# Optimization experiments

Measured on AMD Instinct MI355X. Metric: run time of the kernel, lower is better.

Reference implementation:

```python
import jax, jax.numpy as jnp
import numpy as np

HIDDEN = 1024
HEADS = 16
HEAD_DIM = HIDDEN // HEADS
BATCH = 1
SEQ = 4096
SCALE = 1.0 / np.sqrt(HEAD_DIM)


def setup_inputs() -> dict:
    key = jax.random.key(0)
    ks = jax.random.split(key, 5)
    s = 0.02
    return {
        "hidden_states": jax.random.normal(ks[0], (BATCH, SEQ, HIDDEN), jnp.float32),
        "qkv_w": jax.random.normal(ks[1], (3 * HIDDEN, HIDDEN), jnp.float32) * s,
        "qkv_b": jax.random.normal(ks[2], (3 * HIDDEN,), jnp.float32) * s,
        "out_w": jax.random.normal(ks[3], (HIDDEN, HIDDEN), jnp.float32) * s,
        "out_b": jax.random.normal(ks[4], (HIDDEN,), jnp.float32) * s,
    }


def reference(hidden_states, qkv_w, qkv_b, out_w, out_b):
    B, S, H = hidden_states.shape
    # fused QKV projection (torch Linear: x @ W^T + b)
    qkv = hidden_states @ qkv_w.T + qkv_b              # [B, S, 3H]
    qkv = qkv.reshape(B, S, 3, HEADS, HEAD_DIM)
    qkv = jnp.transpose(qkv, (2, 0, 3, 1, 4))          # [3, B, nh, S, hd]
    q, k, v = qkv[0] * SCALE, qkv[1], qkv[2]
    # ring attention over all KV chunks == full softmax attention
    scores = jnp.einsum('bhqd,bhkd->bhqk', q, k)       # [B, nh, S, S]
    probs = jax.nn.softmax(scores, axis=-1)
    ctx = jnp.einsum('bhqk,bhkd->bhqd', probs, v)      # [B, nh, S, hd]
    ctx = jnp.transpose(ctx, (0, 2, 1, 3)).reshape(B, S, H)
    return ctx @ out_w.T + out_b
```

## Files before the change

### kernel.cpp

```cpp
#include <hip/hip_runtime.h>

#define SEQ 4096
#define HID 1024
#define NHEADS 16
#define HDIM 64
#define QK_SCALE 0.1803368801111204f

typedef float  f32x4 __attribute__((ext_vector_type(4)));
typedef int    i32x4 __attribute__((ext_vector_type(4)));
typedef int    i32x2 __attribute__((ext_vector_type(2)));
typedef __bf16 bf16x8 __attribute__((ext_vector_type(8)));
typedef unsigned short u16;
typedef unsigned int   u32;

static __device__ __forceinline__ u16 f2bf(float f) {
  u32 u = __builtin_bit_cast(u32, f);
  return (u16)((u + 0x7FFFu + ((u >> 16) & 1u)) >> 16);
}
static __device__ __forceinline__ int cvtpk(float lo, float hi) {
  int r;
  asm("v_cvt_pk_bf16_f32 %0, %1, %2" : "=v"(r) : "v"(lo), "v"(hi));
  return r;
}
static __device__ __forceinline__ f32x4 exp2v(f32x4 x) {
  f32x4 o;
  o.x = __builtin_amdgcn_exp2f(x.x);
  o.y = __builtin_amdgcn_exp2f(x.y);
  o.z = __builtin_amdgcn_exp2f(x.z);
  o.w = __builtin_amdgcn_exp2f(x.w);
  return o;
}
static __device__ __forceinline__ float sum4(f32x4 x) {
  return (x.x + x.y) + (x.z + x.w);
}
static __device__ __forceinline__ f32x4 mfma16(i32x4 a, i32x4 b, f32x4 c) {
  return __builtin_amdgcn_mfma_f32_16x16x32_bf16(
      __builtin_bit_cast(bf16x8, a), __builtin_bit_cast(bf16x8, b), c, 0, 0, 0);
}

#define GLD(gsrc, lds_dst)                                        \
  __builtin_amdgcn_global_load_lds(                               \
      (const __attribute__((address_space(1))) void*)(gsrc),      \
      (__attribute__((address_space(3))) void*)(lds_dst), 16, 0, 0)

__global__ __launch_bounds__(256) void cvt_kernel(
    const float* __restrict__ X, const float* __restrict__ Wq,
    const float* __restrict__ Wo, u16* __restrict__ Xb,
    u16* __restrict__ Wqb, u16* __restrict__ Wob) {
  const int u = blockIdx.x * 256 + threadIdx.x;
  const float* src; u16* dst; int local;
  if (u < 524288)       { src = X;  dst = Xb;  local = u; }
  else if (u < 917504)  { src = Wq; dst = Wqb; local = u - 524288; }
  else                  { src = Wo; dst = Wob; local = u - 917504; }
  const int row = local >> 7, gu = local & 127;
  const int w = gu & 7, blk = gu >> 3;
  const int ks = w >> 2, q2 = w & 3;
  const float* s = src + (size_t)row * 1024 + blk * 64 + ks * 32 + q2 * 4;
  float4 x0 = *(const float4*)s;
  float4 x1 = *(const float4*)(s + 16);
  i32x4 o = {cvtpk(x0.x, x0.y), cvtpk(x0.z, x0.w),
             cvtpk(x1.x, x1.y), cvtpk(x1.z, x1.w)};
  *(i32x4*)(dst + (size_t)row * 1024 + blk * 64 + w * 8) = o;
}

static __device__ __forceinline__ void gemm_tile(
    const u16* __restrict__ A, const u16* __restrict__ B,
    int mb, int nb, u16 (*LA)[128][64], u16 (*LB)[128][64],
    f32x4 acc[4][4]) {
  const int t = threadIdx.x, lane = t & 63, wv = t >> 6;
  const int g = lane >> 4, r = lane & 15;
  const int wr = wv >> 1, wc = wv & 1;
  const int lr = lane >> 3, sl = lane & 7;

  const u16* pa = A + (size_t)(mb + wv * 32 + lr) * 1024 + ((sl ^ lr) << 3);
  const u16* pb = B + (size_t)(nb + wv * 32 + lr) * 1024 + ((sl ^ lr) << 3);

  const u16* afp[4][2];
  const u16* bfp[4][2];
#pragma unroll
  for (int i = 0; i < 4; ++i)
#pragma unroll
    for (int ks = 0; ks < 2; ++ks) {
      const int sw = r & 7;
      afp[i][ks] = &LA[0][wr * 64 + i * 16 + r][(((ks * 4 + g) ^ sw) << 3)];
      bfp[i][ks] = &LB[0][wc * 64 + i * 16 + r][(((ks * 4 + g) ^ sw) << 3)];
    }
#pragma unroll
  for (int i = 0; i < 4; ++i)
#pragma unroll
    for (int j = 0; j < 4; ++j) acc[i][j] = (f32x4)0.0f;

#pragma unroll
  for (int j = 0; j < 4; ++j) {
    GLD(pa + j * 8 * 1024, &LA[0][wv * 32 + j * 8][0]);
    GLD(pb + j * 8 * 1024, &LB[0][wv * 32 + j * 8][0]);
  }
  pa += 64; pb += 64;
  __syncthreads();

#define GEMM_STEP(BU, PRE)                                                  \
  {                                                                         \
    if (PRE) {                                                              \
      _Pragma("unroll")                                                     \
      for (int j = 0; j < 4; ++j) {                                         \
        GLD(pa + j * 8 * 1024, &LA[(BU) ^ 1][wv * 32 + j * 8][0]);          \
        GLD(pb + j * 8 * 1024, &LB[(BU) ^ 1][wv * 32 + j * 8][0]);          \
      }                                                                     \
      pa += 64; pb += 64;                                                   \
    }                                                                       \
    i32x4 af[4][2], bf[4][2];                                               \
    _Pragma("unroll")                                                       \
    for (int i = 0; i < 4; ++i)                                             \
      _Pragma("unroll")                                                     \
      for (int ks = 0; ks < 2; ++ks) {                                      \
        af[i][ks] = *(const i32x4*)(afp[i][ks] + (BU) * 8192);              \
        bf[i][ks] = *(const i32x4*)(bfp[i][ks] + (BU) * 8192);              \
      }                                                                     \
    __builtin_amdgcn_s_setprio(1);                                          \
    _Pragma("unroll")                                                       \
    for (int ks = 0; ks < 2; ++ks)                                          \
      _Pragma("unroll")                                                     \
      for (int i = 0; i < 4; ++i)                                           \
        _Pragma("unroll")                                                   \
        for (int j = 0; j < 4; ++j)                                         \
          acc[i][j] = mfma16(af[i][ks], bf[j][ks], acc[i][j]);              \
    __builtin_amdgcn_s_setprio(0);                                          \
    __syncthreads();                                                        \
  }

  for (int kk = 0; kk < 8; ++kk) {
    GEMM_STEP(0, true)
    GEMM_STEP(1, (kk < 7))
  }
#undef GEMM_STEP
}

__global__ __launch_bounds__(256) void qkv_kernel(
    const u16* __restrict__ A, const u16* __restrict__ Bw,
    const float* __restrict__ BI, u16* __restrict__ qws,
    u16* __restrict__ kws, u16* __restrict__ vtws) {
  __shared__ u16 LA[2][128][64];
  __shared__ u16 LB[2][128][64];
  const int t = threadIdx.x, lane = t & 63, wv = t >> 6;
  const int g = lane >> 4, r = lane & 15;
  const int wr = wv >> 1, wc = wv & 1;
  const int mb = blockIdx.x * 128, nb = blockIdx.y * 128;

  f32x4 acc[4][4];
  gemm_tile(A, Bw, mb, nb, LA, LB, acc);

#pragma unroll
  for (int ni = 0; ni < 4; ni++) {
    const int n = nb + wc * 64 + ni * 16 + r;
    const float bias = BI[n];
    const int which = n >> 10;
    const int h = (n >> 6) & 15;
    const int d = n & 63;
    if (which == 2) {
      u16* base = vtws + (((size_t)(h * 64 + d)) << 12) + mb + wr * 64;
#pragma unroll
      for (int mi = 0; mi < 4; mi++) {
#pragma unroll
        for (int e = 0; e < 4; e += 2) {
          float v0 = acc[mi][ni][e] + bias;
          float v1 = acc[mi][ni][e + 1] + bias;
          const int s6 = mi * 16 + g * 4 + e;
          const int pos = (s6 & 32) | (((s6 >> 2) & 3) << 3) |
                          (((s6 >> 4) & 1) << 2) | (s6 & 3);
          *(u32*)(base + pos) = (u32)cvtpk(v0, v1);
        }
      }
    } else {
      u16* dst = which ? kws : qws;
      const float sc = which ? 1.0f : QK_SCALE;
      const int dq = ((d & 32) | (((d >> 2) & 3) << 3) |
                      (((d >> 4) & 1) << 2) | (d & 3));
#pragma unroll
      for (int mi = 0; mi < 4; mi++) {
        const int m0 = mb + wr * 64 + mi * 16 + g * 4;
#pragma unroll
        for (int e = 0; e < 4; e += 2) {
          float v0 = (acc[mi][ni][e] + bias) * sc;
          float v1 = (acc[mi][ni][e + 1] + bias) * sc;
          int w = cvtpk(v0, v1);
          dst[((size_t)h * SEQ + m0 + e) * HDIM + dq] = (u16)w;
          dst[((size_t)h * SEQ + m0 + e + 1) * HDIM + dq] = (u16)(w >> 16);
        }
      }
    }
  }
}

__global__ __launch_bounds__(256, 2) void attn_kernel(
    const u16* __restrict__ qws, const u16* __restrict__ kws,
    const u16* __restrict__ vtws, u16* __restrict__ ctx) {
  __shared__ u16 Kl[2][64][64];
  __shared__ u16 Vtl[2][64][64];
  const int t = threadIdx.x;
  const int lane = t & 63, wv = t >> 6;
  const int g = lane >> 4, r = lane & 15;

  const int fb = blockIdx.x;
  const int swz = (fb & 7) * 64 + (fb >> 3);
  const int h = swz >> 5;
  const int qb = (swz & 31) * 128 + wv * 32;

  i32x4 qf[2][2];
#pragma unroll
  for (int qt = 0; qt < 2; qt++)
#pragma unroll
    for (int db = 0; db < 2; db++)
      qf[qt][db] = *(const i32x4*)(qws +
          ((size_t)(h * SEQ + qb + qt * 16 + r) * HDIM + db * 32 + g * 8));

  f32x4 acc[2][4];
  f32x4 l4[2];
  const f32x4 zero4 = (f32x4)0.0f;
#pragma unroll
  for (int qt = 0; qt < 2; qt++) {
    l4[qt] = (f32x4)0.0f;
#pragma unroll
    for (int dc = 0; dc < 4; dc++) acc[qt][dc] = (f32x4)0.0f;
  }

  const u16* kh_base = kws + (size_t)h * SEQ * HDIM;
  const u16* vt_base = vtws + ((size_t)h << 18);

  const int lr8 = lane >> 3, sl = lane & 7;
  const u16* kgA = kh_base + (size_t)(16 * wv + lr8) * HDIM +
                   ((sl ^ (lr8 & 7)) << 3);
  const u16* kgB = kgA + 8 * HDIM;
  const u16* vtgA = vt_base + (size_t)(16 * wv + lr8) * SEQ +
                    ((sl ^ (lr8 & 7)) << 3);
  const u16* vtgB = vtgA + (size_t)8 * SEQ;

  const u16* kfp0[4];
  const u16* kfp1[4];
  const u16* vfp0[4];
  const u16* vfp1[4];
#pragma unroll
  for (int i = 0; i < 4; ++i) {
    const int R = i * 16 + r;
    const int sw = R & 7;
    kfp0[i] = &Kl[0][R][(g ^ sw) << 3];
    kfp1[i] = &Kl[0][R][((4 + g) ^ sw) << 3];
    vfp0[i] = &Vtl[0][R][(g ^ sw) << 3];
    vfp1[i] = &Vtl[0][R][((4 + g) ^ sw) << 3];
  }

  GLD(kgA, &Kl[0][wv * 16][0]);
  GLD(kgB, &Kl[0][wv * 16 + 8][0]);
  GLD(vtgA, &Vtl[0][wv * 16][0]);
  GLD(vtgB, &Vtl[0][wv * 16 + 8][0]);
  kgA += 4096; kgB += 4096; vtgA += 64; vtgB += 64;
  __syncthreads();

#define ATTN_STEP(B, PRE)                                                   \
  {                                                                         \
    if (PRE) {                                                              \
      GLD(kgA, &Kl[(B) ^ 1][wv * 16][0]);                                   \
      GLD(kgB, &Kl[(B) ^ 1][wv * 16 + 8][0]);                               \
      GLD(vtgA, &Vtl[(B) ^ 1][wv * 16][0]);                                 \
      GLD(vtgB, &Vtl[(B) ^ 1][wv * 16 + 8][0]);                             \
      kgA += 4096; kgB += 4096; vtgA += 64; vtgB += 64;                     \
    }                                                                       \
    f32x4 st[2][4];                                                         \
    __builtin_amdgcn_s_setprio(1);                                          \
    _Pragma("unroll")                                                       \
    for (int kt = 0; kt < 4; ++kt) {                                        \
      i32x4 kf0 = *(const i32x4*)(kfp0[kt] + (B) * 4096);                   \
      i32x4 kf1 = *(const i32x4*)(kfp1[kt] + (B) * 4096);                   \
      st[0][kt] = mfma16(kf0, qf[0][0], zero4);                             \
      st[0][kt] = mfma16(kf1, qf[0][1], st[0][kt]);                         \
      st[1][kt] = mfma16(kf0, qf[1][0], zero4);                             \
      st[1][kt] = mfma16(kf1, qf[1][1], st[1][kt]);                         \
    }                                                                       \
    __builtin_amdgcn_s_setprio(0);                                          \
                          \
    i32x4 pf[2][2];                                                         \
    _Pragma("unroll")                                                       \
    for (int qt = 0; qt < 2; ++qt) {                                        \
      f32x4 p0 = exp2v(st[qt][0]);                                          \
      f32x4 p1 = exp2v(st[qt][1]);                                          \
      f32x4 p2 = exp2v(st[qt][2]);                                          \
      f32x4 p3 = exp2v(st[qt][3]);                                          \
      l4[qt] += p0; l4[qt] += p1; l4[qt] += p2; l4[qt] += p3;               \
      pf[qt][0] = (i32x4){cvtpk(p0.x, p0.y), cvtpk(p0.z, p0.w),             \
                          cvtpk(p1.x, p1.y), cvtpk(p1.z, p1.w)};            \
      pf[qt][1] = (i32x4){cvtpk(p2.x, p2.y), cvtpk(p2.z, p2.w),             \
                          cvtpk(p3.x, p3.y), cvtpk(p3.z, p3.w)};            \
    }                                                                       \
     \
    __builtin_amdgcn_s_setprio(1);                                          \
    _Pragma("unroll")                                                       \
    for (int dc = 0; dc < 4; ++dc) {                                        \
      i32x4 vf0 = *(const i32x4*)(vfp0[dc] + (B) * 4096);                   \
      i32x4 vf1 = *(const i32x4*)(vfp1[dc] + (B) * 4096);                   \
      acc[0][dc] = mfma16(pf[0][0], vf0, acc[0][dc]);                       \
      acc[0][dc] = mfma16(pf[0][1], vf1, acc[0][dc]);                       \
      acc[1][dc] = mfma16(pf[1][0], vf0, acc[1][dc]);                       \
      acc[1][dc] = mfma16(pf[1][1], vf1, acc[1][dc]);                       \
    }                                                                       \
    __builtin_amdgcn_s_setprio(0);                                          \
    __syncthreads();                                                        \
  }

  for (int cc = 0; cc < 32; ++cc) {
    ATTN_STEP(0, true)
    ATTN_STEP(1, (cc < 31))
  }
#undef ATTN_STEP

#pragma unroll
  for (int qt = 0; qt < 2; ++qt) {
    float lsum = sum4(l4[qt]);
    lsum += __shfl_xor(lsum, 16);
    lsum += __shfl_xor(lsum, 32);
#pragma unroll
    for (int rr = 0; rr < 4; ++rr) {
      const float lr_ = __shfl(lsum, 4 * g + rr);
      const float inv = 1.0f / lr_;
      const int s_ = qb + qt * 16 + 4 * g + rr;
#pragma unroll
      for (int dc = 0; dc < 4; ++dc) {
        const int shuf = ((dc >> 1) << 5) | ((r >> 2) << 3) | ((dc & 1) << 2) | (r & 3);
        ctx[(size_t)s_ * HID + h * HDIM + shuf] = f2bf(acc[qt][dc][rr] * inv);
      }
    }
  }
}

__global__ __launch_bounds__(256) void out_kernel(
    const u16* __restrict__ A, const u16* __restrict__ Bw,
    const float* __restrict__ BI, float* __restrict__ out) {
  __shared__ u16 LA[2][128][64];
  __shared__ u16 LB[2][128][64];
  const int t = threadIdx.x, lane = t & 63, wv = t >> 6;
  const int g = lane >> 4, r = lane & 15;
  const int wr = wv >> 1, wc = wv & 1;
  const int mb = blockIdx.x * 128, nb = blockIdx.y * 128;

  f32x4 acc[4][4];
  gemm_tile(A, Bw, mb, nb, LA, LB, acc);

#pragma unroll
  for (int ni = 0; ni < 4; ni++) {
    const int n = nb + wc * 64 + ni * 16 + r;
    const float bias = BI[n];
#pragma unroll
    for (int mi = 0; mi < 4; mi++) {
      const int m0 = mb + wr * 64 + mi * 16 + g * 4;
#pragma unroll
      for (int e = 0; e < 4; e++)
        out[(size_t)(m0 + e) * HID + n] = acc[mi][ni][e] + bias;
    }
  }
}

extern "C" void kernel_launch(void* const* d_in, const int* in_sizes, int n_in,
                              void* d_out, int out_size, void* d_ws, size_t ws_size,
                              hipStream_t stream) {
  const float* X    = (const float*)d_in[0];
  const float* Wqkv = (const float*)d_in[1];
  const float* Bqkv = (const float*)d_in[2];
  const float* Wout = (const float*)d_in[3];
  const float* Bout = (const float*)d_in[4];
  float* out = (float*)d_out;

  const size_t per = (size_t)NHEADS * SEQ * HDIM;
  u16* qws = (u16*)d_ws;
  u16* kws = qws + per;
  u16* vtws = kws + per;
  u16* xbctx = vtws + per;
  u16* wqb = xbctx + per;
  u16* wob = wqb + (size_t)3072 * 1024;

  cvt_kernel<<<4096, 256, 0, stream>>>(X, Wqkv, Wout, xbctx, wqb, wob);
  qkv_kernel<<<dim3(32, 24), 256, 0, stream>>>(xbctx, wqb, Bqkv, qws, kws, vtws);
  attn_kernel<<<dim3(512), 256, 0, stream>>>(qws, kws, vtws, xbctx);
  out_kernel<<<dim3(32, 8), 256, 0, stream>>>(xbctx, wob, Bout, out);
}
```

Before: 138.6 us.

## Software-pipeline QK^T one tile ahead of PV with triple-buffered V

Restructures the attention inner loop so that the QK^T MFMAs for the next KV tile are issued after the PV MFMAs for the current tile. The exp2 and softmax work can then overlap with matrix-core work across iterations. V gets a third shared-memory buffer, a prologue computes the first score tile, and the loop is unrolled by six with explicit buffer rotation. The cost is more live registers (two score arrays) and more LDS, which could lower occupancy under the launch bound of 2 blocks.

```diff
diff --git a/kernel.cpp b/kernel.cpp
--- a/kernel.cpp
+++ b/kernel.cpp
@@ -195,7 +195,7 @@
     const u16* __restrict__ qws, const u16* __restrict__ kws,
     const u16* __restrict__ vtws, u16* __restrict__ ctx) {
   __shared__ u16 Kl[2][64][64];
-  __shared__ u16 Vtl[2][64][64];
+  __shared__ u16 Vtl[3][64][64];
   const int t = threadIdx.x;
   const int lane = t & 63, wv = t >> 6;
   const int g = lane >> 4, r = lane & 15;
@@ -248,68 +248,93 @@
     vfp1[i] = &Vtl[0][R][((4 + g) ^ sw) << 3];
   }
 
+  f32x4 stA[2][4], stB[2][4];
+
   GLD(kgA, &Kl[0][wv * 16][0]);
   GLD(kgB, &Kl[0][wv * 16 + 8][0]);
   GLD(vtgA, &Vtl[0][wv * 16][0]);
   GLD(vtgB, &Vtl[0][wv * 16 + 8][0]);
   kgA += 4096; kgB += 4096; vtgA += 64; vtgB += 64;
+  GLD(kgA, &Kl[1][wv * 16][0]);
+  GLD(kgB, &Kl[1][wv * 16 + 8][0]);
+  GLD(vtgA, &Vtl[1][wv * 16][0]);
+  GLD(vtgB, &Vtl[1][wv * 16 + 8][0]);
+  kgA += 4096; kgB += 4096; vtgA += 64; vtgB += 64;
   __syncthreads();
-
-#define ATTN_STEP(B, PRE)                                                   \
+#pragma unroll
+  for (int kt = 0; kt < 4; ++kt) {
+    i32x4 kf0 = *(const i32x4*)(kfp0[kt]);
+    i32x4 kf1 = *(const i32x4*)(kfp1[kt]);
+    stA[0][kt] = mfma16(kf0, qf[0][0], zero4);
+    stA[0][kt] = mfma16(kf1, qf[0][1], stA[0][kt]);
+    stA[1][kt] = mfma16(kf0, qf[1][0], zero4);
+    stA[1][kt] = mfma16(kf1, qf[1][1], stA[1][kt]);
+  }
+  __syncthreads();
+
+#define ATTN_ITER(KBD, KBQ, VBP, VBD, ST_IN, ST_OUT, DO_DMA, DO_QK)         \
   {                                                                         \
-    if (PRE) {                                                              \
-      GLD(kgA, &Kl[(B) ^ 1][wv * 16][0]);                                   \
-      GLD(kgB, &Kl[(B) ^ 1][wv * 16 + 8][0]);                               \
-      GLD(vtgA, &Vtl[(B) ^ 1][wv * 16][0]);                                 \
-      GLD(vtgB, &Vtl[(B) ^ 1][wv * 16 + 8][0]);                             \
+    if (DO_DMA) {                                                           \
+      GLD(kgA, &Kl[KBD][wv * 16][0]);                                       \
+      GLD(kgB, &Kl[KBD][wv * 16 + 8][0]);                                   \
+      GLD(vtgA, &Vtl[VBD][wv * 16][0]);                                     \
+      GLD(vtgB, &Vtl[VBD][wv * 16 + 8][0]);                                 \
       kgA += 4096; kgB += 4096; vtgA += 64; vtgB += 64;                     \
     }                                                                       \
-    f32x4 st[2][4];                                                         \
-    __builtin_amdgcn_s_setprio(1);                                          \
-    _Pragma("unroll")                                                       \
-    for (int kt = 0; kt < 4; ++kt) {                                        \
-      i32x4 kf0 = *(const i32x4*)(kfp0[kt] + (B) * 4096);                   \
-      i32x4 kf1 = *(const i32x4*)(kfp1[kt] + (B) * 4096);                   \
-      st[0][kt] = mfma16(kf0, qf[0][0], zero4);                             \
-      st[0][kt] = mfma16(kf1, qf[0][1], st[0][kt]);                         \
-      st[1][kt] = mfma16(kf0, qf[1][0], zero4);                             \
-      st[1][kt] = mfma16(kf1, qf[1][1], st[1][kt]);                         \
-    }                                                                       \
-    __builtin_amdgcn_s_setprio(0);                                          \
-                          \
+                                   \
     i32x4 pf[2][2];                                                         \
     _Pragma("unroll")                                                       \
     for (int qt = 0; qt < 2; ++qt) {                                        \
-      f32x4 p0 = exp2v(st[qt][0]);                                          \
-      f32x4 p1 = exp2v(st[qt][1]);                                          \
-      f32x4 p2 = exp2v(st[qt][2]);                                          \
-      f32x4 p3 = exp2v(st[qt][3]);                                          \
+      f32x4 p0 = exp2v(ST_IN[qt][0]);                                       \
+      f32x4 p1 = exp2v(ST_IN[qt][1]);                                       \
+      f32x4 p2 = exp2v(ST_IN[qt][2]);                                       \
+      f32x4 p3 = exp2v(ST_IN[qt][3]);                                       \
       l4[qt] += p0; l4[qt] += p1; l4[qt] += p2; l4[qt] += p3;               \
       pf[qt][0] = (i32x4){cvtpk(p0.x, p0.y), cvtpk(p0.z, p0.w),             \
                           cvtpk(p1.x, p1.y), cvtpk(p1.z, p1.w)};            \
       pf[qt][1] = (i32x4){cvtpk(p2.x, p2.y), cvtpk(p2.z, p2.w),             \
                           cvtpk(p3.x, p3.y), cvtpk(p3.z, p3.w)};            \
     }                                                                       \
-     \
     __builtin_amdgcn_s_setprio(1);                                          \
+                                                   \
     _Pragma("unroll")                                                       \
     for (int dc = 0; dc < 4; ++dc) {                                        \
-      i32x4 vf0 = *(const i32x4*)(vfp0[dc] + (B) * 4096);                   \
-      i32x4 vf1 = *(const i32x4*)(vfp1[dc] + (B) * 4096);                   \
+      i32x4 vf0 = *(const i32x4*)(vfp0[dc] + (VBP) * 4096);                 \
+      i32x4 vf1 = *(const i32x4*)(vfp1[dc] + (VBP) * 4096);                 \
       acc[0][dc] = mfma16(pf[0][0], vf0, acc[0][dc]);                       \
       acc[0][dc] = mfma16(pf[0][1], vf1, acc[0][dc]);                       \
       acc[1][dc] = mfma16(pf[1][0], vf0, acc[1][dc]);                       \
       acc[1][dc] = mfma16(pf[1][1], vf1, acc[1][dc]);                       \
     }                                                                       \
+           \
+    if (DO_QK) {                                                            \
+      _Pragma("unroll")                                                     \
+      for (int kt = 0; kt < 4; ++kt) {                                      \
+        i32x4 kf0 = *(const i32x4*)(kfp0[kt] + (KBQ) * 4096);               \
+        i32x4 kf1 = *(const i32x4*)(kfp1[kt] + (KBQ) * 4096);               \
+        ST_OUT[0][kt] = mfma16(kf0, qf[0][0], zero4);                       \
+        ST_OUT[0][kt] = mfma16(kf1, qf[0][1], ST_OUT[0][kt]);               \
+        ST_OUT[1][kt] = mfma16(kf0, qf[1][0], zero4);                       \
+        ST_OUT[1][kt] = mfma16(kf1, qf[1][1], ST_OUT[1][kt]);               \
+      }                                                                     \
+    }                                                                       \
     __builtin_amdgcn_s_setprio(0);                                          \
     __syncthreads();                                                        \
   }
 
-  for (int cc = 0; cc < 32; ++cc) {
-    ATTN_STEP(0, true)
-    ATTN_STEP(1, (cc < 31))
-  }
-#undef ATTN_STEP
+  for (int cc = 0; cc < 10; ++cc) {
+    ATTN_ITER(0, 1, 0, 2, stA, stB, true, true)
+    ATTN_ITER(1, 0, 1, 0, stB, stA, true, true)
+    ATTN_ITER(0, 1, 2, 1, stA, stB, true, true)
+    ATTN_ITER(1, 0, 0, 2, stB, stA, true, true)
+    ATTN_ITER(0, 1, 1, 0, stA, stB, true, true)
+    ATTN_ITER(1, 0, 2, 1, stB, stA, true, true)
+  }
+  ATTN_ITER(0, 1, 0, 2, stA, stB, true, true)
+  ATTN_ITER(1, 0, 1, 0, stB, stA, true, true)
+  ATTN_ITER(0, 1, 2, 1, stA, stB, false, true)
+  ATTN_ITER(1, 0, 0, 2, stB, stA, false, false)
+#undef ATTN_ITER
 
 #pragma unroll
   for (int qt = 0; qt < 2; ++qt) {
```

New measurement: 135.1 us, median of 2. 1.03x faster.

## Software-pipeline attention loop with 3-stage K and 4-stage V LDS buffers

Applied to the files above, without the earlier changes.

Restructures the attention main loop into a software pipeline. The QK^T MFMAs for the next chunk are issued after the PV MFMAs of the current chunk, so the exp/convert work overlaps with matrix work. K and V LDS buffers grow to 3 and 4 stages with prefetch depth two, and the generic __syncthreads is replaced by explicit vmcnt waits plus s_barrier. This is meant to hide global-load latency and barrier stalls. It raises LDS use and register pressure (two score arrays live at once), which may cut occupancy, and the hand-indexed buffer rotation is easy to get wrong.

```diff
diff --git a/kernel.cpp b/kernel.cpp
--- a/kernel.cpp
+++ b/kernel.cpp
@@ -194,8 +194,8 @@
 __global__ __launch_bounds__(256, 2) void attn_kernel(
     const u16* __restrict__ qws, const u16* __restrict__ kws,
     const u16* __restrict__ vtws, u16* __restrict__ ctx) {
-  __shared__ u16 Kl[2][64][64];
-  __shared__ u16 Vtl[2][64][64];
+  __shared__ u16 Kl[3][64][64];
+  __shared__ u16 Vtl[4][64][64];
   const int t = threadIdx.x;
   const int lane = t & 63, wv = t >> 6;
   const int g = lane >> 4, r = lane & 15;
@@ -248,68 +248,95 @@
     vfp1[i] = &Vtl[0][R][((4 + g) ^ sw) << 3];
   }
 
-  GLD(kgA, &Kl[0][wv * 16][0]);
-  GLD(kgB, &Kl[0][wv * 16 + 8][0]);
-  GLD(vtgA, &Vtl[0][wv * 16][0]);
-  GLD(vtgB, &Vtl[0][wv * 16 + 8][0]);
+  f32x4 stA[2][4], stB[2][4];
+
+#define SYNCC(N)                                                            \
+  asm volatile("s_waitcnt vmcnt(" #N ") lgkmcnt(0)" ::: "memory");          \
+  __builtin_amdgcn_sched_barrier(0);                                        \
+  __builtin_amdgcn_s_barrier();                                             \
+  __builtin_amdgcn_sched_barrier(0);                                        \
+  asm volatile("" ::: "memory");
+
+#define DMA_CH(KB, VB)                                                      \
+  GLD(kgA, &Kl[KB][wv * 16][0]);                                            \
+  GLD(kgB, &Kl[KB][wv * 16 + 8][0]);                                        \
+  GLD(vtgA, &Vtl[VB][wv * 16][0]);                                          \
+  GLD(vtgB, &Vtl[VB][wv * 16 + 8][0]);                                      \
   kgA += 4096; kgB += 4096; vtgA += 64; vtgB += 64;
-  __syncthreads();
-
-#define ATTN_STEP(B, PRE)                                                   \
+
+#define QKC(KB, ST)                                                         \
+  _Pragma("unroll")                                                         \
+  for (int kt = 0; kt < 4; ++kt) {                                          \
+    i32x4 kf0 = *(const i32x4*)(kfp0[kt] + (KB) * 4096);                    \
+    i32x4 kf1 = *(const i32x4*)(kfp1[kt] + (KB) * 4096);                    \
+    ST[0][kt] = mfma16(kf0, qf[0][0], zero4);                               \
+    ST[0][kt] = mfma16(kf1, qf[0][1], ST[0][kt]);                           \
+    ST[1][kt] = mfma16(kf0, qf[1][0], zero4);                               \
+    ST[1][kt] = mfma16(kf1, qf[1][1], ST[1][kt]);                           \
+  }
+
+  DMA_CH(0, 0)
+  DMA_CH(1, 1)
+  DMA_CH(2, 2)
+  SYNCC(8)
+  QKC(0, stA)
+  SYNCC(4)
+
+#define ATTN_ITER(KD, VD, VBP, KBQ, STI, STO, DO_DMA, DO_QK)                \
   {                                                                         \
-    if (PRE) {                                                              \
-      GLD(kgA, &Kl[(B) ^ 1][wv * 16][0]);                                   \
-      GLD(kgB, &Kl[(B) ^ 1][wv * 16 + 8][0]);                               \
-      GLD(vtgA, &Vtl[(B) ^ 1][wv * 16][0]);                                 \
-      GLD(vtgB, &Vtl[(B) ^ 1][wv * 16 + 8][0]);                             \
-      kgA += 4096; kgB += 4096; vtgA += 64; vtgB += 64;                     \
-    }                                                                       \
-    f32x4 st[2][4];                                                         \
-    __builtin_amdgcn_s_setprio(1);                                          \
-    _Pragma("unroll")                                                       \
-    for (int kt = 0; kt < 4; ++kt) {                                        \
-      i32x4 kf0 = *(const i32x4*)(kfp0[kt] + (B) * 4096);                   \
-      i32x4 kf1 = *(const i32x4*)(kfp1[kt] + (B) * 4096);                   \
-      st[0][kt] = mfma16(kf0, qf[0][0], zero4);                             \
-      st[0][kt] = mfma16(kf1, qf[0][1], st[0][kt]);                         \
-      st[1][kt] = mfma16(kf0, qf[1][0], zero4);                             \
-      st[1][kt] = mfma16(kf1, qf[1][1], st[1][kt]);                         \
-    }                                                                       \
-    __builtin_amdgcn_s_setprio(0);                                          \
-                          \
+    if (DO_DMA) { DMA_CH(KD, VD) }                                          \
+                                     \
     i32x4 pf[2][2];                                                         \
     _Pragma("unroll")                                                       \
     for (int qt = 0; qt < 2; ++qt) {                                        \
-      f32x4 p0 = exp2v(st[qt][0]);                                          \
-      f32x4 p1 = exp2v(st[qt][1]);                                          \
-      f32x4 p2 = exp2v(st[qt][2]);                                          \
-      f32x4 p3 = exp2v(st[qt][3]);                                          \
+      f32x4 p0 = exp2v(STI[qt][0]);                                         \
+      f32x4 p1 = exp2v(STI[qt][1]);                                         \
+      f32x4 p2 = exp2v(STI[qt][2]);                                         \
+      f32x4 p3 = exp2v(STI[qt][3]);                                         \
       l4[qt] += p0; l4[qt] += p1; l4[qt] += p2; l4[qt] += p3;               \
       pf[qt][0] = (i32x4){cvtpk(p0.x, p0.y), cvtpk(p0.z, p0.w),             \
                           cvtpk(p1.x, p1.y), cvtpk(p1.z, p1.w)};            \
       pf[qt][1] = (i32x4){cvtpk(p2.x, p2.y), cvtpk(p2.z, p2.w),             \
                           cvtpk(p3.x, p3.y), cvtpk(p3.z, p3.w)};            \
     }                                                                       \
-     \
     __builtin_amdgcn_s_setprio(1);                                          \
+                                                   \
     _Pragma("unroll")                                                       \
     for (int dc = 0; dc < 4; ++dc) {                                        \
-      i32x4 vf0 = *(const i32x4*)(vfp0[dc] + (B) * 4096);                   \
-      i32x4 vf1 = *(const i32x4*)(vfp1[dc] + (B) * 4096);                   \
+      i32x4 vf0 = *(const i32x4*)(vfp0[dc] + (VBP) * 4096);                 \
+      i32x4 vf1 = *(const i32x4*)(vfp1[dc] + (VBP) * 4096);                 \
       acc[0][dc] = mfma16(pf[0][0], vf0, acc[0][dc]);                       \
       acc[0][dc] = mfma16(pf[0][1], vf1, acc[0][dc]);                       \
       acc[1][dc] = mfma16(pf[1][0], vf0, acc[1][dc]);                       \
       acc[1][dc] = mfma16(pf[1][1], vf1, acc[1][dc]);                       \
     }                                                                       \
+              \
+    if (DO_QK) { QKC(KBQ, STO) }                                            \
     __builtin_amdgcn_s_setprio(0);                                          \
-    __syncthreads();                                                        \
-  }
-
-  for (int cc = 0; cc < 32; ++cc) {
-    ATTN_STEP(0, true)
-    ATTN_STEP(1, (cc < 31))
-  }
-#undef ATTN_STEP
+  }
+
+  for (int cc = 0; cc < 5; ++cc) {
+    ATTN_ITER(0, 3, 0, 1, stA, stB, true, true) SYNCC(4)
+    ATTN_ITER(1, 0, 1, 2, stB, stA, true, true) SYNCC(4)
+    ATTN_ITER(2, 1, 2, 0, stA, stB, true, true) SYNCC(4)
+    ATTN_ITER(0, 2, 3, 1, stB, stA, true, true) SYNCC(4)
+    ATTN_ITER(1, 3, 0, 2, stA, stB, true, true) SYNCC(4)
+    ATTN_ITER(2, 0, 1, 0, stB, stA, true, true) SYNCC(4)
+    ATTN_ITER(0, 1, 2, 1, stA, stB, true, true) SYNCC(4)
+    ATTN_ITER(1, 2, 3, 2, stB, stA, true, true) SYNCC(4)
+    ATTN_ITER(2, 3, 0, 0, stA, stB, true, true) SYNCC(4)
+    ATTN_ITER(0, 0, 1, 1, stB, stA, true, true) SYNCC(4)
+    ATTN_ITER(1, 1, 2, 2, stA, stB, true, true) SYNCC(4)
+    ATTN_ITER(2, 2, 3, 0, stB, stA, true, true) SYNCC(4)
+  }
+  ATTN_ITER(0, 3, 0, 1, stA, stB, true, true) SYNCC(4)
+  ATTN_ITER(0, 0, 1, 2, stB, stA, false, true) SYNCC(0)
+  ATTN_ITER(0, 0, 2, 0, stA, stB, false, true)
+  ATTN_ITER(0, 0, 3, 0, stB, stA, false, false)
+#undef ATTN_ITER
+#undef QKC
+#undef DMA_CH
+#undef SYNCC
 
 #pragma unroll
   for (int qt = 0; qt < 2; ++qt) {
```

New measurement: 135.2 us. 1.02x faster.

## Double KV chunk size per attention iteration to halve barriers

Applied to the files above, without the earlier changes.

Each attention iteration now processes 128 keys instead of 64. K and V^T shared tiles double in size, and the direct-to-LDS load pattern and swizzle are rewritten for the wider V^T rows. This halves the number of __syncthreads and loop iterations and gives each barrier interval more MFMA work to overlap with the prefetch. In exchange it doubles LDS use per block and raises register pressure from the larger score and probability fragments, which may hurt occupancy under launch_bounds(256,2).

```diff
diff --git a/kernel.cpp b/kernel.cpp
--- a/kernel.cpp
+++ b/kernel.cpp
@@ -194,8 +194,8 @@
 __global__ __launch_bounds__(256, 2) void attn_kernel(
     const u16* __restrict__ qws, const u16* __restrict__ kws,
     const u16* __restrict__ vtws, u16* __restrict__ ctx) {
-  __shared__ u16 Kl[2][64][64];
-  __shared__ u16 Vtl[2][64][64];
+  __shared__ u16 Kl[2][128][64];
+  __shared__ u16 Vtl[2][64][128];
   const int t = threadIdx.x;
   const int lane = t & 63, wv = t >> 6;
   const int g = lane >> 4, r = lane & 15;
@@ -226,90 +226,87 @@
   const u16* kh_base = kws + (size_t)h * SEQ * HDIM;
   const u16* vt_base = vtws + ((size_t)h << 18);
 
-  const int lr8 = lane >> 3, sl = lane & 7;
-  const u16* kgA = kh_base + (size_t)(16 * wv + lr8) * HDIM +
-                   ((sl ^ (lr8 & 7)) << 3);
-  const u16* kgB = kgA + 8 * HDIM;
-  const u16* vtgA = vt_base + (size_t)(16 * wv + lr8) * SEQ +
-                    ((sl ^ (lr8 & 7)) << 3);
-  const u16* vtgB = vtgA + (size_t)8 * SEQ;
-
-  const u16* kfp0[4];
-  const u16* kfp1[4];
-  const u16* vfp0[4];
-  const u16* vfp1[4];
-#pragma unroll
-  for (int i = 0; i < 4; ++i) {
-    const int R = i * 16 + r;
-    const int sw = R & 7;
-    kfp0[i] = &Kl[0][R][(g ^ sw) << 3];
-    kfp1[i] = &Kl[0][R][((4 + g) ^ sw) << 3];
-    vfp0[i] = &Vtl[0][R][(g ^ sw) << 3];
-    vfp1[i] = &Vtl[0][R][((4 + g) ^ sw) << 3];
-  }
-
-  GLD(kgA, &Kl[0][wv * 16][0]);
-  GLD(kgB, &Kl[0][wv * 16 + 8][0]);
-  GLD(vtgA, &Vtl[0][wv * 16][0]);
-  GLD(vtgB, &Vtl[0][wv * 16 + 8][0]);
-  kgA += 4096; kgB += 4096; vtgA += 64; vtgB += 64;
+  const u16* kgA = kh_base + (size_t)(32 * wv + (lane >> 3)) * HDIM +
+                   (((lane & 7) ^ ((lane >> 3) & 7)) << 3);
+  const u16* vg[4];
+#pragma unroll
+  for (int j = 0; j < 4; ++j)
+    vg[j] = vt_base + (size_t)(16 * wv + 4 * j + (lane >> 4)) * SEQ +
+            (((lane & 15) ^ (4 * j + (lane >> 4))) << 3);
+
+  const u16* kb0 = &Kl[0][0][0] + r * 64 + ((g ^ (r & 7)) << 3);
+  const u16* kb1 = &Kl[0][0][0] + r * 64 + (((4 + g) ^ (r & 7)) << 3);
+  const u16* vb[4];
+#pragma unroll
+  for (int m = 0; m < 4; ++m)
+    vb[m] = &Vtl[0][0][0] + r * 128 + (((4 * m + g) ^ r) << 3);
+
+#define DMA_CH(B)                                                           \
+  {                                                                         \
+    _Pragma("unroll")                                                       \
+    for (int j = 0; j < 4; ++j) {                                           \
+      GLD(kgA + j * 512, &Kl[B][32 * wv + 8 * j][0]);                       \
+      GLD(vg[j], &Vtl[B][16 * wv + 4 * j][0]);                              \
+    }                                                                       \
+    kgA += 8192;                                                            \
+    _Pragma("unroll")                                                       \
+    for (int j = 0; j < 4; ++j) vg[j] += 128;                               \
+  }
+
+  DMA_CH(0)
   __syncthreads();
 
-#define ATTN_STEP(B, PRE)                                                   \
+#define ATTN_ITER(B, PRE)                                                   \
   {                                                                         \
-    if (PRE) {                                                              \
-      GLD(kgA, &Kl[(B) ^ 1][wv * 16][0]);                                   \
-      GLD(kgB, &Kl[(B) ^ 1][wv * 16 + 8][0]);                               \
-      GLD(vtgA, &Vtl[(B) ^ 1][wv * 16][0]);                                 \
-      GLD(vtgB, &Vtl[(B) ^ 1][wv * 16 + 8][0]);                             \
-      kgA += 4096; kgB += 4096; vtgA += 64; vtgB += 64;                     \
-    }                                                                       \
-    f32x4 st[2][4];                                                         \
+    if (PRE) { DMA_CH((B) ^ 1) }                                            \
+    f32x4 st[2][8];                                                         \
     __builtin_amdgcn_s_setprio(1);                                          \
     _Pragma("unroll")                                                       \
-    for (int kt = 0; kt < 4; ++kt) {                                        \
-      i32x4 kf0 = *(const i32x4*)(kfp0[kt] + (B) * 4096);                   \
-      i32x4 kf1 = *(const i32x4*)(kfp1[kt] + (B) * 4096);                   \
+    for (int kt = 0; kt < 8; ++kt) {                                        \
+      i32x4 kf0 = *(const i32x4*)(kb0 + kt * 1024 + (B) * 8192);            \
+      i32x4 kf1 = *(const i32x4*)(kb1 + kt * 1024 + (B) * 8192);            \
       st[0][kt] = mfma16(kf0, qf[0][0], zero4);                             \
       st[0][kt] = mfma16(kf1, qf[0][1], st[0][kt]);                         \
       st[1][kt] = mfma16(kf0, qf[1][0], zero4);                             \
       st[1][kt] = mfma16(kf1, qf[1][1], st[1][kt]);                         \
     }                                                                       \
     __builtin_amdgcn_s_setprio(0);                                          \
-                          \
-    i32x4 pf[2][2];                                                         \
+              \
+    i32x4 pf[2][4];                                                         \
     _Pragma("unroll")                                                       \
     for (int qt = 0; qt < 2; ++qt) {                                        \
-      f32x4 p0 = exp2v(st[qt][0]);                                          \
-      f32x4 p1 = exp2v(st[qt][1]);                                          \
-      f32x4 p2 = exp2v(st[qt][2]);                                          \
-      f32x4 p3 = exp2v(st[qt][3]);                                          \
-      l4[qt] += p0; l4[qt] += p1; l4[qt] += p2; l4[qt] += p3;               \
-      pf[qt][0] = (i32x4){cvtpk(p0.x, p0.y), cvtpk(p0.z, p0.w),             \
-                          cvtpk(p1.x, p1.y), cvtpk(p1.z, p1.w)};            \
-      pf[qt][1] = (i32x4){cvtpk(p2.x, p2.y), cvtpk(p2.z, p2.w),             \
-                          cvtpk(p3.x, p3.y), cvtpk(p3.z, p3.w)};            \
-    }                                                                       \
-     \
+      _Pragma("unroll")                                                     \
+      for (int m = 0; m < 4; ++m) {                                         \
+        f32x4 pa = exp2v(st[qt][2 * m]);                                    \
+        f32x4 pb = exp2v(st[qt][2 * m + 1]);                                \
+        l4[qt] += pa; l4[qt] += pb;                                         \
+        pf[qt][m] = (i32x4){cvtpk(pa.x, pa.y), cvtpk(pa.z, pa.w),           \
+                            cvtpk(pb.x, pb.y), cvtpk(pb.z, pb.w)};          \
+      }                                                                     \
+    }                                                                       \
+              \
     __builtin_amdgcn_s_setprio(1);                                          \
     _Pragma("unroll")                                                       \
     for (int dc = 0; dc < 4; ++dc) {                                        \
-      i32x4 vf0 = *(const i32x4*)(vfp0[dc] + (B) * 4096);                   \
-      i32x4 vf1 = *(const i32x4*)(vfp1[dc] + (B) * 4096);                   \
-      acc[0][dc] = mfma16(pf[0][0], vf0, acc[0][dc]);                       \
-      acc[0][dc] = mfma16(pf[0][1], vf1, acc[0][dc]);                       \
-      acc[1][dc] = mfma16(pf[1][0], vf0, acc[1][dc]);                       \
-      acc[1][dc] = mfma16(pf[1][1], vf1, acc[1][dc]);                       \
+      _Pragma("unroll")                                                     \
+      for (int m = 0; m < 4; ++m) {                                         \
+        i32x4 vf = *(const i32x4*)(vb[m] + dc * 2048 + (B) * 8192);         \
+        acc[0][dc] = mfma16(pf[0][m], vf, acc[0][dc]);                      \
+        acc[1][dc] = mfma16(pf[1][m], vf, acc[1][dc]);                      \
+      }                                                                     \
     }                                                                       \
     __builtin_amdgcn_s_setprio(0);                                          \
     __syncthreads();                                                        \
   }
 
-  for (int cc = 0; cc < 32; ++cc) {
-    ATTN_STEP(0, true)
-    ATTN_STEP(1, (cc < 31))
-  }
-#undef ATTN_STEP
+  for (int cc = 0; cc < 15; ++cc) {
+    ATTN_ITER(0, true)
+    ATTN_ITER(1, true)
+  }
+  ATTN_ITER(0, true)
+  ATTN_ITER(1, false)
+#undef ATTN_ITER
+#undef DMA_CH
 
 #pragma unroll
   for (int qt = 0; qt < 2; ++qt) {
```

Measured after the change: 138.0 us. No clear change (-0.4%).
